# Kernel tuning notes

Hardware: AMD Instinct MI355X
Metric: run time of the kernel (lower is better)

## Reference

```python
import jax, jax.numpy as jnp
import numpy as np

N, E, F_IN, G, C = 100000, 3200000, 64, 1024, 10
BN_EPS = 1e-5


def _glorot(key, shape):
    fan_in, fan_out = shape[0], shape[1]
    lim = jnp.sqrt(6.0 / (fan_in + fan_out))
    return jax.random.uniform(key, shape, jnp.float32, -lim, lim)


def setup_inputs() -> dict:
    key = jax.random.key(0)
    ks = jax.random.split(key, 20)
    x = jax.random.normal(ks[0], (N, F_IN), jnp.float32)
    edge_index = jax.random.randint(ks[1], (2, E), 0, N, jnp.int64)
    batch = jnp.sort(jax.random.randint(ks[2], (N,), 0, G, jnp.int64))
    p = {
        'W1a': _glorot(ks[3], (F_IN, 128)), 'b1a': jnp.zeros((128,), jnp.float32),
        'W1b': _glorot(ks[4], (128, 128)), 'b1b': jnp.zeros((128,), jnp.float32),
        'g1': jnp.ones((128,), jnp.float32), 'be1': jnp.zeros((128,), jnp.float32),
        'W2a': _glorot(ks[5], (128, 64)), 'b2a': jnp.zeros((64,), jnp.float32),
        'W2b': _glorot(ks[6], (64, 64)), 'b2b': jnp.zeros((64,), jnp.float32),
        'g2': jnp.ones((64,), jnp.float32), 'be2': jnp.zeros((64,), jnp.float32),
        'W3a': _glorot(ks[7], (64, 32)), 'b3a': jnp.zeros((32,), jnp.float32),
        'W3b': _glorot(ks[8], (32, 32)), 'b3b': jnp.zeros((32,), jnp.float32),
        'g3': jnp.ones((32,), jnp.float32), 'be3': jnp.zeros((32,), jnp.float32),
        'Wf1': _glorot(ks[9], (32, 128)), 'bf1': jnp.zeros((128,), jnp.float32),
        'Wf2': _glorot(ks[10], (128, 64)), 'bf2': jnp.zeros((64,), jnp.float32),
        'Wf3': _glorot(ks[11], (64, C)), 'bf3': jnp.zeros((C,), jnp.float32),
    }
    return {'x': x, 'edge_index': edge_index, 'batch': batch, **p}


def _gin(x, src, dst, Wa, ba, Wb, bb):
    # GINConv (eps=0): h = MLP(x + sum_{j->i} x_j)
    agg = jax.ops.segment_sum(x[src], dst, num_segments=N)
    h = jax.nn.relu((x + agg) @ Wa + ba)
    return h @ Wb + bb


def _bn(x, g, b):
    # BatchNorm1d, training-mode batch statistics (biased variance)
    mu = jnp.mean(x, axis=0)
    var = jnp.mean((x - mu) ** 2, axis=0)
    return (x - mu) * jax.lax.rsqrt(var + BN_EPS) * g + b


def reference(x, edge_index, batch,
              W1a, b1a, W1b, b1b, g1, be1,
              W2a, b2a, W2b, b2b, g2, be2,
              W3a, b3a, W3b, b3b, g3, be3,
              Wf1, bf1, Wf2, bf2, Wf3, bf3):
    src, dst = edge_index[0], edge_index[1]
    z = _bn(jax.nn.relu(_gin(x, src, dst, W1a, b1a, W1b, b1b)), g1, be1)
    z = _bn(jax.nn.relu(_gin(z, src, dst, W2a, b2a, W2b, b2b)), g2, be2)
    z = _bn(jax.nn.relu(_gin(z, src, dst, W3a, b3a, W3b, b3b)), g3, be3)
    # global_add_pool over graph ids
    z = jax.ops.segment_sum(z, batch, num_segments=G)  # [G, 32]
    cr = jax.nn.relu(z @ Wf1 + bf1)
    cr = jax.nn.relu(cr @ Wf2 + bf2)  # dropout = identity (eval)
    cr = cr @ Wf3 + bf3
    return cr.reshape(-1, C)
```

## Files before the change

kernel.cpp:

```cpp
#include <hip/hip_runtime.h>

#define BN_EPS 1e-5f

typedef _Float16 f16;
typedef _Float16 f16x8 __attribute__((ext_vector_type(8)));
typedef _Float16 f16x4 __attribute__((ext_vector_type(4)));
typedef float f32x4 __attribute__((ext_vector_type(4)));

#define NBLK 512
#define BSHIFT 8
#define BMASK 255

__device__ __forceinline__ void wfrag_one(const float* __restrict__ W, f16* __restrict__ out,
        int FIN, int FOUT, int f,
        const float* __restrict__ stats, const float* __restrict__ g, float invN) {
    int j = f & 7;
    int lane = (f >> 3) & 63;
    int tile = f >> 9;
    int NT = FOUT >> 4;
    int t = tile % NT, s = tile / NT;
    int k = s * 32 + (lane >> 4) * 8 + j;
    int n = t * 16 + (lane & 15);
    float w = W[(size_t)k * FOUT + n];
    if (stats) {
        float mu = stats[k] * invN;
        float var = fmaxf(stats[FIN + k] * invN - mu * mu, 0.0f);
        w *= rsqrtf(var + BN_EPS) * g[k];
    }
    out[f] = (f16)w;
}

__global__ __launch_bounds__(256) void setup_count(const float4* __restrict__ x,
        f16x4* __restrict__ xh, int n4,
        const float* __restrict__ W1a, f16* __restrict__ Wh1a,
        const float* __restrict__ W1b, f16* __restrict__ Wh1b,
        const float* __restrict__ W2b, f16* __restrict__ Wh2b,
        const float* __restrict__ W3b, f16* __restrict__ Wh3b,
        const int* __restrict__ dst, int* __restrict__ hist,
        int NBK, int CHUNK, int E) {
    __shared__ int lh[512];
    const int BC = (n4 + 255) / 256;
    int bid = blockIdx.x;
    const int t = threadIdx.x;
    if (bid < BC) {
        int i = bid * 256 + t;
        if (i < n4) {
            float4 v = x[i];
            f16x4 o;
            o.x = (f16)v.x; o.y = (f16)v.y; o.z = (f16)v.z; o.w = (f16)v.w;
            xh[i] = o;
        }
        return;
    }
    bid -= BC;
    if (bid < 116) {
        if (bid < 32)       wfrag_one(W1a, Wh1a, 64, 128, bid * 256 + t, nullptr, nullptr, 0.f);
        else if (bid < 96)  wfrag_one(W1b, Wh1b, 128, 128, (bid - 32) * 256 + t, nullptr, nullptr, 0.f);
        else if (bid < 112) wfrag_one(W2b, Wh2b, 64, 64, (bid - 96) * 256 + t, nullptr, nullptr, 0.f);
        else                wfrag_one(W3b, Wh3b, 32, 32, (bid - 112) * 256 + t, nullptr, nullptr, 0.f);
        return;
    }
    const int blk = bid - 116;
    for (int r = t; r < 512; r += 256) lh[r] = 0;
    __syncthreads();
    const int e0 = blk * CHUNK, e1 = min(E, e0 + CHUNK);
    const int nq = (e1 - e0) >> 2;
    const int4* d4 = (const int4*)(dst + e0);
    for (int q = t; q < nq; q += 256) {
        int4 v = d4[q];
        atomicAdd(&lh[v.x >> BSHIFT], 1);
        atomicAdd(&lh[v.y >> BSHIFT], 1);
        atomicAdd(&lh[v.z >> BSHIFT], 1);
        atomicAdd(&lh[v.w >> BSHIFT], 1);
    }
    for (int e = e0 + (nq << 2) + t; e < e1; e += 256) atomicAdd(&lh[dst[e] >> BSHIFT], 1);
    __syncthreads();
    for (int r = t; r < NBK; r += 256) hist[r * NBLK + blk] = lh[r];
}

__global__ __launch_bounds__(512) void bkt_bscan(int* __restrict__ hist,
        int* __restrict__ btot) {
    __shared__ int sh[512];
    const int b = blockIdx.x, t = threadIdx.x;
    int v = hist[b * NBLK + t];
    sh[t] = v;
    __syncthreads();
    for (int d = 1; d < 512; d <<= 1) {
        int u = (t >= d) ? sh[t - d] : 0;
        __syncthreads();
        sh[t] += u;
        __syncthreads();
    }
    hist[b * NBLK + t] = sh[t] - v;
    if (t == 511) btot[b] = sh[511];
}

__global__ __launch_bounds__(512) void bkt_scatter(const int* __restrict__ src,
        const int* __restrict__ dst, const int* __restrict__ hist,
        const int* __restrict__ btot, int* __restrict__ bucketed,
        int NBK, int CHUNK, int E) {
    __shared__ int sc[512];
    __shared__ int lc[512];
    const int blk = blockIdx.x, t = threadIdx.x;
    int v = (t < NBK) ? btot[t] : 0;
    sc[t] = v;
    __syncthreads();
    for (int d = 1; d < 512; d <<= 1) {
        int u = (t >= d) ? sc[t - d] : 0;
        __syncthreads();
        sc[t] += u;
        __syncthreads();
    }
    if (t < NBK) lc[t] = (sc[t] - v) + hist[t * NBLK + blk];
    __syncthreads();
    const int e0 = blk * CHUNK, e1 = min(E, e0 + CHUNK);
    const int nq = (e1 - e0) >> 2;
    const int4* d4 = (const int4*)(dst + e0);
    const int4* s4 = (const int4*)(src + e0);
    for (int q = t; q < nq; q += 512) {
        int4 d = d4[q];
        int4 s = s4[q];
        int sl;
        sl = atomicAdd(&lc[d.x >> BSHIFT], 1); bucketed[sl] = ((d.x & BMASK) << 18) | s.x;
        sl = atomicAdd(&lc[d.y >> BSHIFT], 1); bucketed[sl] = ((d.y & BMASK) << 18) | s.y;
        sl = atomicAdd(&lc[d.z >> BSHIFT], 1); bucketed[sl] = ((d.z & BMASK) << 18) | s.z;
        sl = atomicAdd(&lc[d.w >> BSHIFT], 1); bucketed[sl] = ((d.w & BMASK) << 18) | s.w;
    }
    for (int e = e0 + (nq << 2) + t; e < e1; e += 512) {
        int d = dst[e];
        int slot = atomicAdd(&lc[d >> BSHIFT], 1);
        bucketed[slot] = ((d & BMASK) << 18) | src[e];
    }
}

__global__ __launch_bounds__(512) void bkt_csr(const int* __restrict__ bucketed,
        const int* __restrict__ btot, int* __restrict__ off,
        int* __restrict__ elist, int NBK, int N, int E) {
    __shared__ int sc[512];
    __shared__ int lh[256];
    __shared__ int lc[256];
    __shared__ int sh[256];
    const int b = blockIdx.x, t = threadIdx.x;
    int v = (t < NBK) ? btot[t] : 0;
    sc[t] = v;
    __syncthreads();
    for (int d = 1; d < 512; d <<= 1) {
        int u = (t >= d) ? sc[t - d] : 0;
        __syncthreads();
        sc[t] += u;
        __syncthreads();
    }
    const int cnt  = btot[b];
    const int base = sc[b] - cnt;
    if (b == 0 && t == 0) off[N] = E;
    const int b0 = b << BSHIFT;
    const int R = min(N - b0, 256);
    if (t < 256) lh[t] = 0;
    __syncthreads();
    for (int i = t; i < cnt; i += 512) atomicAdd(&lh[bucketed[base + i] >> 18], 1);
    __syncthreads();
    int v0 = 0;
    if (t < 256) { v0 = lh[t]; sh[t] = v0; }
    __syncthreads();
    for (int d = 1; d < 256; d <<= 1) {
        int u = 0;
        if (t < 256 && t >= d) u = sh[t - d];
        __syncthreads();
        if (t < 256) sh[t] += u;
        __syncthreads();
    }
    if (t < 256) { int ex = sh[t] - v0; lh[t] = ex; lc[t] = ex; }
    __syncthreads();
    if (t < R) off[b0 + t] = base + lh[t];
    for (int i = t; i < cnt; i += 512) {
        int p = bucketed[base + i];
        int rk = atomicAdd(&lc[p >> 18], 1);
        elist[base + rk] = p & 0x3FFFF;
    }
}

template<int F, bool AFFINE>
__global__ __launch_bounds__(256) void gather_v(const int* __restrict__ off,
        const int* __restrict__ elist, const f16* __restrict__ in,
        f16* __restrict__ out, const float* __restrict__ v,
        const float* __restrict__ bias, int N) {
    constexpr int TPN = F / 8;
    constexpr int NPB = 256 / TPN;
    const int i = blockIdx.x * NPB + threadIdx.x / TPN;
    const int l = threadIdx.x & (TPN - 1);
    if (i >= N) return;
    const int j0 = l * 8;
    const f16x8* __restrict__ inv = (const f16x8*)in;
    f16x8 s = inv[(size_t)i * TPN + l];
    float a[8];
#pragma unroll
    for (int u = 0; u < 8; u++) a[u] = (float)s[u];
    int k = off[i], e = off[i + 1];
    const float cnt = (float)(e - k + 1);
    f16x8 c0, c1, c2, c3;
    if (k + 4 <= e) {
        c0 = inv[(size_t)elist[k + 0] * TPN + l];
        c1 = inv[(size_t)elist[k + 1] * TPN + l];
        c2 = inv[(size_t)elist[k + 2] * TPN + l];
        c3 = inv[(size_t)elist[k + 3] * TPN + l];
        k += 4;
        for (; k + 4 <= e; k += 4) {
            f16x8 d0 = inv[(size_t)elist[k + 0] * TPN + l];
            f16x8 d1 = inv[(size_t)elist[k + 1] * TPN + l];
            f16x8 d2 = inv[(size_t)elist[k + 2] * TPN + l];
            f16x8 d3 = inv[(size_t)elist[k + 3] * TPN + l];
#pragma unroll
            for (int u = 0; u < 8; u++)
                a[u] += ((float)c0[u] + (float)c1[u]) + ((float)c2[u] + (float)c3[u]);
            c0 = d0; c1 = d1; c2 = d2; c3 = d3;
        }
#pragma unroll
        for (int u = 0; u < 8; u++)
            a[u] += ((float)c0[u] + (float)c1[u]) + ((float)c2[u] + (float)c3[u]);
    }
    for (; k < e; k++) {
        f16x8 p = inv[(size_t)elist[k] * TPN + l];
#pragma unroll
        for (int u = 0; u < 8; u++) a[u] += (float)p[u];
    }
    if (AFFINE) {
        float4 vv0 = *(const float4*)(v + j0);
        float4 vv1 = *(const float4*)(v + j0 + 4);
        float4 bb0 = *(const float4*)(bias + j0);
        float4 bb1 = *(const float4*)(bias + j0 + 4);
        a[0] = fmaxf(fmaf(cnt, vv0.x, a[0] + bb0.x), 0.0f);
        a[1] = fmaxf(fmaf(cnt, vv0.y, a[1] + bb0.y), 0.0f);
        a[2] = fmaxf(fmaf(cnt, vv0.z, a[2] + bb0.z), 0.0f);
        a[3] = fmaxf(fmaf(cnt, vv0.w, a[3] + bb0.w), 0.0f);
        a[4] = fmaxf(fmaf(cnt, vv1.x, a[4] + bb1.x), 0.0f);
        a[5] = fmaxf(fmaf(cnt, vv1.y, a[5] + bb1.y), 0.0f);
        a[6] = fmaxf(fmaf(cnt, vv1.z, a[6] + bb1.z), 0.0f);
        a[7] = fmaxf(fmaf(cnt, vv1.w, a[7] + bb1.w), 0.0f);
    }
    f16x8 o;
#pragma unroll
    for (int u = 0; u < 8; u++) o[u] = (f16)a[u];
    ((f16x8*)(out))[(size_t)i * TPN + l] = o;
}

__global__ __launch_bounds__(256) void layerprep_kernel(const float* __restrict__ W,
        f16* __restrict__ Wh, int FIN, int FOUT,
        const float* __restrict__ stats, const float* __restrict__ g,
        const float* __restrict__ be, float* __restrict__ v, float invN) {
    if (blockIdx.x == 0) {
        int j = threadIdx.x;
        if (j >= FOUT) return;
        float acc = 0.0f;
        for (int k = 0; k < FIN; k++) {
            float mu = stats[k] * invN;
            float var = fmaxf(stats[FIN + k] * invN - mu * mu, 0.0f);
            float sc = rsqrtf(var + BN_EPS) * g[k];
            float sh = be[k] - mu * sc;
            acc = fmaf(sh, W[(size_t)k * FOUT + j], acc);
        }
        v[j] = acc;
        return;
    }
    int f = (blockIdx.x - 1) * 256 + threadIdx.x;
    if (f < FIN * FOUT) wfrag_one(W, Wh, FIN, FOUT, f, stats, g, invN);
}

template<int FIN, int FOUT, int CT, bool STATS, bool RELU, bool BIAS, typename OutT>
__global__ __launch_bounds__(256) void gemm_mfma(const f16* __restrict__ A,
        const f16* __restrict__ Wf, const float* __restrict__ bias,
        OutT* __restrict__ Out, float* __restrict__ stats, int N) {
    constexpr int NS = FIN / 32;
    constexpr int NTF = FOUT / 16;
    constexpr int NT = CT / 16;
    constexpr int NCB = FOUT / CT;
    __shared__ float Ss[STATS ? 2 * CT : 1];
    if (STATS) {
        for (int i = threadIdx.x; i < 2 * CT; i += 256) Ss[i] = 0.0f;
        __syncthreads();
    }
    const int cb = blockIdx.x % NCB;
    const int rb = blockIdx.x / NCB;
    const int RB = gridDim.x / NCB;
    const int t0 = cb * NT;
    const int wid = threadIdx.x >> 6;
    const int lane = threadIdx.x & 63;
    const int col = lane & 15;
    const int quad = lane >> 4;

    f16x8 Bf[NS][NT];
#pragma unroll
    for (int s = 0; s < NS; s++)
#pragma unroll
        for (int t = 0; t < NT; t++)
            Bf[s][t] = *(const f16x8*)&Wf[((s * NTF + t0 + t) << 9) + (lane << 3)];

    float bj[NT];
#pragma unroll
    for (int t = 0; t < NT; t++) bj[t] = BIAS ? bias[(t0 + t) * 16 + col] : 0.0f;

    float ls[NT], ls2[NT];
#pragma unroll
    for (int t = 0; t < NT; t++) { ls[t] = 0.0f; ls2[t] = 0.0f; }

    const int S = N >> 4;
    for (int sidx = rb * 4 + wid; sidx < S; sidx += RB * 4) {
        const int m0 = sidx << 4;
        const f16* a0 = A + (size_t)(m0 + col) * FIN + (quad << 3);
        f16x8 Af[NS];
#pragma unroll
        for (int s = 0; s < NS; s++) Af[s] = *(const f16x8*)(a0 + s * 32);
        f32x4 acc[NT];
#pragma unroll
        for (int t = 0; t < NT; t++) acc[t] = (f32x4){bj[t], bj[t], bj[t], bj[t]};
#pragma unroll
        for (int t = 0; t < NT; t++)
#pragma unroll
            for (int s = 0; s < NS; s++)
                acc[t] = __builtin_amdgcn_mfma_f32_16x16x32_f16(Af[s], Bf[s][t], acc[t], 0, 0, 0);
#pragma unroll
        for (int t = 0; t < NT; t++) {
            float v0 = acc[t][0], v1 = acc[t][1], v2 = acc[t][2], v3 = acc[t][3];
            if (RELU) {
                v0 = fmaxf(v0, 0.0f); v1 = fmaxf(v1, 0.0f);
                v2 = fmaxf(v2, 0.0f); v3 = fmaxf(v3, 0.0f);
            }
            if (STATS) {
                ls[t]  += (v0 + v1) + (v2 + v3);
                ls2[t] += (v0 * v0 + v1 * v1) + (v2 * v2 + v3 * v3);
            }
            OutT* o = Out + (size_t)(m0 + quad * 4) * FOUT + (t0 + t) * 16 + col;
            o[0]        = (OutT)v0;
            o[FOUT]     = (OutT)v1;
            o[2 * FOUT] = (OutT)v2;
            o[3 * FOUT] = (OutT)v3;
        }
    }

    if (STATS) {
#pragma unroll
        for (int t = 0; t < NT; t++) {
            float s1 = ls[t], s2 = ls2[t];
            s1 += __shfl_xor(s1, 16); s1 += __shfl_xor(s1, 32);
            s2 += __shfl_xor(s2, 16); s2 += __shfl_xor(s2, 32);
            if (quad == 0) {
                atomicAdd(&Ss[t * 16 + col], s1);
                atomicAdd(&Ss[CT + t * 16 + col], s2);
            }
        }
        __syncthreads();
        for (int i = threadIdx.x; i < CT; i += 256) {
            atomicAdd(&stats[cb * CT + i], Ss[i]);
            atomicAdd(&stats[FOUT + cb * CT + i], Ss[CT + i]);
        }
    }
}

__global__ __launch_bounds__(256) void bn_pool_kernel(const float* __restrict__ y,
        const float* __restrict__ stats, const float* __restrict__ gw,
        const float* __restrict__ bw, const int* __restrict__ batch,
        float* __restrict__ pool, int N, float invN) {
    constexpr int F = 32, CH = 64;
    int q = threadIdx.x >> 5;
    int j = threadIdx.x & 31;
    int r0 = (blockIdx.x * 8 + q) * CH;
    if (r0 >= N) return;
    int r1 = min(r0 + CH, N);
    float mu = stats[j] * invN;
    float var = fmaxf(stats[F + j] * invN - mu * mu, 0.0f);
    float sc = rsqrtf(var + BN_EPS) * gw[j];
    float sh = bw[j] - mu * sc;
    int curg = batch[r0];
    float acc = 0.0f;
    for (int r = r0; r < r1; r++) {
        int g = batch[r];
        if (g != curg) {
            atomicAdd(pool + (size_t)curg * 32 + j, acc);
            acc = 0.0f;
            curg = g;
        }
        acc = fmaf(y[(size_t)r * 32 + j], sc, sh + acc);
    }
    atomicAdd(pool + (size_t)curg * 32 + j, acc);
}

__global__ __launch_bounds__(128) void fc_kernel(const float* __restrict__ pool,
        const float* __restrict__ Wf1, const float* __restrict__ bf1,
        const float* __restrict__ Wf2, const float* __restrict__ bf2,
        const float* __restrict__ Wf3, const float* __restrict__ bf3,
        float* __restrict__ out) {
    __shared__ float zin[32];
    __shared__ float h1[128];
    __shared__ float h2[64];
    const int gidx = blockIdx.x;
    const int t = threadIdx.x;
    if (t < 32) zin[t] = pool[(size_t)gidx * 32 + t];
    __syncthreads();
    {
        float a = bf1[t];
        for (int k = 0; k < 32; k++) a = fmaf(zin[k], Wf1[k * 128 + t], a);
        h1[t] = fmaxf(a, 0.0f);
    }
    __syncthreads();
    if (t < 64) {
        float a = bf2[t];
        for (int k = 0; k < 128; k++) a = fmaf(h1[k], Wf2[k * 64 + t], a);
        h2[t] = fmaxf(a, 0.0f);
    }
    __syncthreads();
    if (t < 10) {
        float a = bf3[t];
        for (int k = 0; k < 64; k++) a = fmaf(h2[k], Wf3[k * 10 + t], a);
        out[(size_t)gidx * 10 + t] = a;
    }
}

extern "C" void kernel_launch(void* const* d_in, const int* in_sizes, int n_in,
                              void* d_out, int out_size, void* d_ws, size_t ws_size,
                              hipStream_t stream) {
    const float* x   = (const float*)d_in[0];
    const int*  ei   = (const int*)d_in[1];
    const int*  batch= (const int*)d_in[2];
    const float* W1a = (const float*)d_in[3];  const float* b1a = (const float*)d_in[4];
    const float* W1b = (const float*)d_in[5];  const float* b1b = (const float*)d_in[6];
    const float* g1  = (const float*)d_in[7];  const float* be1 = (const float*)d_in[8];
    const float* W2a = (const float*)d_in[9];  const float* b2a = (const float*)d_in[10];
    const float* W2b = (const float*)d_in[11]; const float* b2b = (const float*)d_in[12];
    const float* g2  = (const float*)d_in[13]; const float* be2 = (const float*)d_in[14];
    const float* W3a = (const float*)d_in[15]; const float* b3a = (const float*)d_in[16];
    const float* W3b = (const float*)d_in[17]; const float* b3b = (const float*)d_in[18];
    const float* g3  = (const float*)d_in[19]; const float* be3 = (const float*)d_in[20];
    const float* Wf1 = (const float*)d_in[21]; const float* bf1 = (const float*)d_in[22];
    const float* Wf2 = (const float*)d_in[23]; const float* bf2 = (const float*)d_in[24];
    const float* Wf3 = (const float*)d_in[25]; const float* bf3 = (const float*)d_in[26];

    const int N = in_sizes[2];
    const int E = in_sizes[1] / 2;
    const int G = out_size / 10;
    const int* src = ei;
    const int* dst = ei + E;

    const int NBK = (N + BMASK) >> BSHIFT;
    const int CHUNK = (((E + NBLK - 1) / NBLK) + 3) & ~3;

    float* B0   = (float*)d_ws;
    float* B1   = B0 + (size_t)N * 128;
    float* pool = B1 + (size_t)N * 128;
    float* st1  = pool + (size_t)G * 32;
    float* st2  = st1 + 256;
    float* st3  = st2 + 256;
    int* off    = (int*)(st3 + 256);
    int* elist  = off + (N + 1);
    float* v2   = (float*)(elist + E);
    float* v3   = v2 + 64;
    int* btot   = (int*)(v3 + 32);
    f16* Wh1a   = (f16*)(btot + NBK);
    f16* Wh1b   = Wh1a + 64 * 128;
    f16* Wh2a   = Wh1b + 128 * 128;
    f16* Wh2b   = Wh2a + 128 * 64;
    f16* Wh3a   = Wh2b + 64 * 64;
    f16* Wh3b   = Wh3a + 64 * 32;

    int* bucketed = (int*)B1;
    int* hist     = bucketed + E;

    f16* xh    = (f16*)B0;
    f16* A1    = (f16*)B1;
    f16* H1    = (f16*)B0 + (size_t)N * 64;
    f16* Y1    = (f16*)B1 + (size_t)N * 64;
    f16* Z1    = (f16*)B0;
    f16* H2    = (f16*)B1;
    f16* Y2    = (f16*)B0 + (size_t)N * 64;
    f16* Z2    = (f16*)B0;
    f16* H3    = (f16*)B1;
    float* Y3  = B1 + (size_t)N * 64;

    hipMemsetAsync(pool, 0, ((size_t)G * 32 + 768) * sizeof(float), stream);

    const float invN = 1.0f / (float)N;
    const int GG = 640;

    {
        int BC = (N * 16 + 255) / 256;
        setup_count<<<BC + 116 + NBLK, 256, 0, stream>>>(
            (const float4*)x, (f16x4*)xh, N * 16,
            W1a, Wh1a, W1b, Wh1b, W2b, Wh2b, W3b, Wh3b,
            dst, hist, NBK, CHUNK, E);
    }

    bkt_bscan  <<<NBK, 512, 0, stream>>>(hist, btot);
    bkt_scatter<<<NBLK, 512, 0, stream>>>(src, dst, hist, btot, bucketed, NBK, CHUNK, E);
    bkt_csr    <<<NBK, 512, 0, stream>>>(bucketed, btot, off, elist, NBK, N, E);

    gather_v<64, false><<<(N + 31) / 32, 256, 0, stream>>>(off, elist, xh, A1, nullptr, nullptr, N);
    gemm_mfma<64, 128, 64, false, true, true, f16><<<GG, 256, 0, stream>>>(A1, Wh1a, b1a, H1, nullptr, N);
    gemm_mfma<128, 128, 64, true, true, true, f16><<<GG, 256, 0, stream>>>(H1, Wh1b, b1b, Y1, st1, N);

    layerprep_kernel<<<33, 256, 0, stream>>>(W2a, Wh2a, 128, 64, st1, g1, be1, v2, invN);
    gemm_mfma<128, 64, 64, false, false, false, f16><<<GG, 256, 0, stream>>>(Y1, Wh2a, nullptr, Z1, nullptr, N);
    gather_v<64, true><<<(N + 31) / 32, 256, 0, stream>>>(off, elist, Z1, H2, v2, b2a, N);
    gemm_mfma<64, 64, 64, true, true, true, f16><<<GG, 256, 0, stream>>>(H2, Wh2b, b2b, Y2, st2, N);

    layerprep_kernel<<<9, 256, 0, stream>>>(W3a, Wh3a, 64, 32, st2, g2, be2, v3, invN);
    gemm_mfma<64, 32, 32, false, false, false, f16><<<GG, 256, 0, stream>>>(Y2, Wh3a, nullptr, Z2, nullptr, N);
    gather_v<32, true><<<(N + 63) / 64, 256, 0, stream>>>(off, elist, Z2, H3, v3, b3a, N);
    gemm_mfma<32, 32, 32, true, true, true, float><<<GG, 256, 0, stream>>>(H3, Wh3b, b3b, Y3, st3, N);

    bn_pool_kernel<<<(N + 511) / 512, 256, 0, stream>>>(Y3, st3, g3, be3, batch, pool, N, invN);

    fc_kernel<<<G, 128, 0, stream>>>(pool, Wf1, bf1, Wf2, bf2, Wf3, bf3, (float*)d_out);
}
```

Before: 515.6 us.

## Fuse neighbor gather with following MFMA GEMM through shared memory

Each aggregation kernel now does its gather into an LDS tile and immediately runs the next MFMA GEMM on it (with bias, ReLU and optional BN statistics), so the intermediate H arrays are never written to or read back from global memory. BN statistics are spread over 8 copies chosen by block index to cut global atomic contention, and the consumers sum the copies. The cost is more LDS and registers per block, which may lower occupancy for the latency-bound gather.

```diff
diff --git a/kernel.cpp b/kernel.cpp
--- a/kernel.cpp
+++ b/kernel.cpp
@@ -13,7 +13,7 @@
 
 __device__ __forceinline__ void wfrag_one(const float* __restrict__ W, f16* __restrict__ out,
         int FIN, int FOUT, int f,
-        const float* __restrict__ stats, const float* __restrict__ g, float invN) {
+        const float* __restrict__ stats, int NC, const float* __restrict__ g, float invN) {
     int j = f & 7;
     int lane = (f >> 3) & 63;
     int tile = f >> 9;
@@ -23,8 +23,13 @@
     int n = t * 16 + (lane & 15);
     float w = W[(size_t)k * FOUT + n];
     if (stats) {
-        float mu = stats[k] * invN;
-        float var = fmaxf(stats[FIN + k] * invN - mu * mu, 0.0f);
+        float s1 = 0.0f, s2 = 0.0f;
+        for (int c = 0; c < NC; c++) {
+            s1 += stats[c * 2 * FIN + k];
+            s2 += stats[c * 2 * FIN + FIN + k];
+        }
+        float mu = s1 * invN;
+        float var = fmaxf(s2 * invN - mu * mu, 0.0f);
         w *= rsqrtf(var + BN_EPS) * g[k];
     }
     out[f] = (f16)w;
@@ -54,10 +59,10 @@
     }
     bid -= BC;
     if (bid < 116) {
-        if (bid < 32)       wfrag_one(W1a, Wh1a, 64, 128, bid * 256 + t, nullptr, nullptr, 0.f);
-        else if (bid < 96)  wfrag_one(W1b, Wh1b, 128, 128, (bid - 32) * 256 + t, nullptr, nullptr, 0.f);
-        else if (bid < 112) wfrag_one(W2b, Wh2b, 64, 64, (bid - 96) * 256 + t, nullptr, nullptr, 0.f);
-        else                wfrag_one(W3b, Wh3b, 32, 32, (bid - 112) * 256 + t, nullptr, nullptr, 0.f);
+        if (bid < 32)       wfrag_one(W1a, Wh1a, 64, 128, bid * 256 + t, nullptr, 1, nullptr, 0.f);
+        else if (bid < 96)  wfrag_one(W1b, Wh1b, 128, 128, (bid - 32) * 256 + t, nullptr, 1, nullptr, 0.f);
+        else if (bid < 112) wfrag_one(W2b, Wh2b, 64, 64, (bid - 96) * 256 + t, nullptr, 1, nullptr, 0.f);
+        else                wfrag_one(W3b, Wh3b, 32, 32, (bid - 112) * 256 + t, nullptr, 1, nullptr, 0.f);
         return;
     }
     const int blk = bid - 116;
@@ -179,81 +184,159 @@
     }
 }
 
-template<int F, bool AFFINE>
-__global__ __launch_bounds__(256) void gather_v(const int* __restrict__ off,
+template<int F, int FOUT, bool STATS, bool AFFINE, typename OutT>
+__global__ __launch_bounds__(256) void gather_gemm(const int* __restrict__ off,
         const int* __restrict__ elist, const f16* __restrict__ in,
-        f16* __restrict__ out, const float* __restrict__ v,
-        const float* __restrict__ bias, int N) {
+        const f16* __restrict__ Wf, const float* __restrict__ bias,
+        const float* __restrict__ av, const float* __restrict__ ab,
+        OutT* __restrict__ Out, float* __restrict__ stats, int N) {
     constexpr int TPN = F / 8;
     constexpr int NPB = 256 / TPN;
-    const int i = blockIdx.x * NPB + threadIdx.x / TPN;
+    constexpr int SPB = NPB / 16;
+    constexpr int WPS = 4 / SPB;
+    constexpr int NTF = FOUT / 16;
+    constexpr int NTW = NTF / WPS;
+    constexpr int NS = F / 32;
+    constexpr int LDW = F + 8;
+    __shared__ f16 Hl[NPB * LDW];
+    __shared__ float Ss[STATS ? 2 * FOUT : 1];
+    if (STATS) for (int z = threadIdx.x; z < 2 * FOUT; z += 256) Ss[z] = 0.0f;
+
+    const int base = blockIdx.x * NPB;
+    const int rl = threadIdx.x / TPN;
+    const int i = base + rl;
     const int l = threadIdx.x & (TPN - 1);
-    if (i >= N) return;
-    const int j0 = l * 8;
-    const f16x8* __restrict__ inv = (const f16x8*)in;
-    f16x8 s = inv[(size_t)i * TPN + l];
-    float a[8];
-#pragma unroll
-    for (int u = 0; u < 8; u++) a[u] = (float)s[u];
-    int k = off[i], e = off[i + 1];
-    const float cnt = (float)(e - k + 1);
-    f16x8 c0, c1, c2, c3;
-    if (k + 4 <= e) {
-        c0 = inv[(size_t)elist[k + 0] * TPN + l];
-        c1 = inv[(size_t)elist[k + 1] * TPN + l];
-        c2 = inv[(size_t)elist[k + 2] * TPN + l];
-        c3 = inv[(size_t)elist[k + 3] * TPN + l];
-        k += 4;
-        for (; k + 4 <= e; k += 4) {
-            f16x8 d0 = inv[(size_t)elist[k + 0] * TPN + l];
-            f16x8 d1 = inv[(size_t)elist[k + 1] * TPN + l];
-            f16x8 d2 = inv[(size_t)elist[k + 2] * TPN + l];
-            f16x8 d3 = inv[(size_t)elist[k + 3] * TPN + l];
+    if (i < N) {
+        const int j0 = l * 8;
+        const f16x8* __restrict__ inv = (const f16x8*)in;
+        f16x8 s = inv[(size_t)i * TPN + l];
+        float a[8];
+#pragma unroll
+        for (int u = 0; u < 8; u++) a[u] = (float)s[u];
+        int k = off[i], e = off[i + 1];
+        const float cnt = (float)(e - k + 1);
+        f16x8 c0, c1, c2, c3;
+        if (k + 4 <= e) {
+            c0 = inv[(size_t)elist[k + 0] * TPN + l];
+            c1 = inv[(size_t)elist[k + 1] * TPN + l];
+            c2 = inv[(size_t)elist[k + 2] * TPN + l];
+            c3 = inv[(size_t)elist[k + 3] * TPN + l];
+            k += 4;
+            for (; k + 4 <= e; k += 4) {
+                f16x8 d0 = inv[(size_t)elist[k + 0] * TPN + l];
+                f16x8 d1 = inv[(size_t)elist[k + 1] * TPN + l];
+                f16x8 d2 = inv[(size_t)elist[k + 2] * TPN + l];
+                f16x8 d3 = inv[(size_t)elist[k + 3] * TPN + l];
+#pragma unroll
+                for (int u = 0; u < 8; u++)
+                    a[u] += ((float)c0[u] + (float)c1[u]) + ((float)c2[u] + (float)c3[u]);
+                c0 = d0; c1 = d1; c2 = d2; c3 = d3;
+            }
 #pragma unroll
             for (int u = 0; u < 8; u++)
                 a[u] += ((float)c0[u] + (float)c1[u]) + ((float)c2[u] + (float)c3[u]);
-            c0 = d0; c1 = d1; c2 = d2; c3 = d3;
-        }
-#pragma unroll
-        for (int u = 0; u < 8; u++)
-            a[u] += ((float)c0[u] + (float)c1[u]) + ((float)c2[u] + (float)c3[u]);
-    }
-    for (; k < e; k++) {
-        f16x8 p = inv[(size_t)elist[k] * TPN + l];
-#pragma unroll
-        for (int u = 0; u < 8; u++) a[u] += (float)p[u];
-    }
-    if (AFFINE) {
-        float4 vv0 = *(const float4*)(v + j0);
-        float4 vv1 = *(const float4*)(v + j0 + 4);
-        float4 bb0 = *(const float4*)(bias + j0);
-        float4 bb1 = *(const float4*)(bias + j0 + 4);
-        a[0] = fmaxf(fmaf(cnt, vv0.x, a[0] + bb0.x), 0.0f);
-        a[1] = fmaxf(fmaf(cnt, vv0.y, a[1] + bb0.y), 0.0f);
-        a[2] = fmaxf(fmaf(cnt, vv0.z, a[2] + bb0.z), 0.0f);
-        a[3] = fmaxf(fmaf(cnt, vv0.w, a[3] + bb0.w), 0.0f);
-        a[4] = fmaxf(fmaf(cnt, vv1.x, a[4] + bb1.x), 0.0f);
-        a[5] = fmaxf(fmaf(cnt, vv1.y, a[5] + bb1.y), 0.0f);
-        a[6] = fmaxf(fmaf(cnt, vv1.z, a[6] + bb1.z), 0.0f);
-        a[7] = fmaxf(fmaf(cnt, vv1.w, a[7] + bb1.w), 0.0f);
-    }
-    f16x8 o;
-#pragma unroll
-    for (int u = 0; u < 8; u++) o[u] = (f16)a[u];
-    ((f16x8*)(out))[(size_t)i * TPN + l] = o;
+        }
+        for (; k < e; k++) {
+            f16x8 p = inv[(size_t)elist[k] * TPN + l];
+#pragma unroll
+            for (int u = 0; u < 8; u++) a[u] += (float)p[u];
+        }
+        if (AFFINE) {
+            float4 vv0 = *(const float4*)(av + j0);
+            float4 vv1 = *(const float4*)(av + j0 + 4);
+            float4 bb0 = *(const float4*)(ab + j0);
+            float4 bb1 = *(const float4*)(ab + j0 + 4);
+            a[0] = fmaxf(fmaf(cnt, vv0.x, a[0] + bb0.x), 0.0f);
+            a[1] = fmaxf(fmaf(cnt, vv0.y, a[1] + bb0.y), 0.0f);
+            a[2] = fmaxf(fmaf(cnt, vv0.z, a[2] + bb0.z), 0.0f);
+            a[3] = fmaxf(fmaf(cnt, vv0.w, a[3] + bb0.w), 0.0f);
+            a[4] = fmaxf(fmaf(cnt, vv1.x, a[4] + bb1.x), 0.0f);
+            a[5] = fmaxf(fmaf(cnt, vv1.y, a[5] + bb1.y), 0.0f);
+            a[6] = fmaxf(fmaf(cnt, vv1.z, a[6] + bb1.z), 0.0f);
+            a[7] = fmaxf(fmaf(cnt, vv1.w, a[7] + bb1.w), 0.0f);
+        }
+        f16x8 o;
+#pragma unroll
+        for (int u = 0; u < 8; u++) o[u] = (f16)a[u];
+        *(f16x8*)&Hl[rl * LDW + j0] = o;
+    }
+    __syncthreads();
+
+    const int wid = threadIdx.x >> 6;
+    const int lane = threadIdx.x & 63;
+    const int col = lane & 15;
+    const int quad = lane >> 4;
+    const int sid = wid / WPS;
+    const int cg = wid % WPS;
+    const int m0 = base + sid * 16;
+    if (m0 < N) {
+        f16x8 Bf[NS][NTW];
+#pragma unroll
+        for (int s = 0; s < NS; s++)
+#pragma unroll
+            for (int t = 0; t < NTW; t++)
+                Bf[s][t] = *(const f16x8*)&Wf[((s * NTF + cg * NTW + t) << 9) + (lane << 3)];
+        f32x4 acc[NTW];
+#pragma unroll
+        for (int t = 0; t < NTW; t++) {
+            float b = bias[(cg * NTW + t) * 16 + col];
+            acc[t] = (f32x4){b, b, b, b};
+        }
+        f16x8 Af[NS];
+        const int rbase = (sid * 16 + col) * LDW + quad * 8;
+#pragma unroll
+        for (int s = 0; s < NS; s++) Af[s] = *(const f16x8*)&Hl[rbase + s * 32];
+#pragma unroll
+        for (int t = 0; t < NTW; t++)
+#pragma unroll
+            for (int s = 0; s < NS; s++)
+                acc[t] = __builtin_amdgcn_mfma_f32_16x16x32_f16(Af[s], Bf[s][t], acc[t], 0, 0, 0);
+#pragma unroll
+        for (int t = 0; t < NTW; t++) {
+            float v0 = fmaxf(acc[t][0], 0.0f);
+            float v1 = fmaxf(acc[t][1], 0.0f);
+            float v2 = fmaxf(acc[t][2], 0.0f);
+            float v3 = fmaxf(acc[t][3], 0.0f);
+            OutT* o = Out + (size_t)(m0 + quad * 4) * FOUT + (cg * NTW + t) * 16 + col;
+            o[0]        = (OutT)v0;
+            o[FOUT]     = (OutT)v1;
+            o[2 * FOUT] = (OutT)v2;
+            o[3 * FOUT] = (OutT)v3;
+            if (STATS) {
+                float s1 = (v0 + v1) + (v2 + v3);
+                float s2 = (v0 * v0 + v1 * v1) + (v2 * v2 + v3 * v3);
+                s1 += __shfl_xor(s1, 16); s1 += __shfl_xor(s1, 32);
+                s2 += __shfl_xor(s2, 16); s2 += __shfl_xor(s2, 32);
+                if (quad == 0) {
+                    atomicAdd(&Ss[(cg * NTW + t) * 16 + col], s1);
+                    atomicAdd(&Ss[FOUT + (cg * NTW + t) * 16 + col], s2);
+                }
+            }
+        }
+    }
+    if (STATS) {
+        __syncthreads();
+        float* stc = stats + (blockIdx.x & 7) * 2 * FOUT;
+        for (int z = threadIdx.x; z < 2 * FOUT; z += 256) atomicAdd(&stc[z], Ss[z]);
+    }
 }
 
 __global__ __launch_bounds__(256) void layerprep_kernel(const float* __restrict__ W,
         f16* __restrict__ Wh, int FIN, int FOUT,
-        const float* __restrict__ stats, const float* __restrict__ g,
+        const float* __restrict__ stats, int NC, const float* __restrict__ g,
         const float* __restrict__ be, float* __restrict__ v, float invN) {
     if (blockIdx.x == 0) {
         int j = threadIdx.x;
         if (j >= FOUT) return;
         float acc = 0.0f;
         for (int k = 0; k < FIN; k++) {
-            float mu = stats[k] * invN;
-            float var = fmaxf(stats[FIN + k] * invN - mu * mu, 0.0f);
+            float s1 = 0.0f, s2 = 0.0f;
+            for (int c = 0; c < NC; c++) {
+                s1 += stats[c * 2 * FIN + k];
+                s2 += stats[c * 2 * FIN + FIN + k];
+            }
+            float mu = s1 * invN;
+            float var = fmaxf(s2 * invN - mu * mu, 0.0f);
             float sc = rsqrtf(var + BN_EPS) * g[k];
             float sh = be[k] - mu * sc;
             acc = fmaf(sh, W[(size_t)k * FOUT + j], acc);
@@ -262,7 +345,7 @@
         return;
     }
     int f = (blockIdx.x - 1) * 256 + threadIdx.x;
-    if (f < FIN * FOUT) wfrag_one(W, Wh, FIN, FOUT, f, stats, g, invN);
+    if (f < FIN * FOUT) wfrag_one(W, Wh, FIN, FOUT, f, stats, NC, g, invN);
 }
 
 template<int FIN, int FOUT, int CT, bool STATS, bool RELU, bool BIAS, typename OutT>
@@ -356,7 +439,7 @@
 }
 
 __global__ __launch_bounds__(256) void bn_pool_kernel(const float* __restrict__ y,
-        const float* __restrict__ stats, const float* __restrict__ gw,
+        const float* __restrict__ stats, int NC, const float* __restrict__ gw,
         const float* __restrict__ bw, const int* __restrict__ batch,
         float* __restrict__ pool, int N, float invN) {
     constexpr int F = 32, CH = 64;
@@ -365,8 +448,13 @@
     int r0 = (blockIdx.x * 8 + q) * CH;
     if (r0 >= N) return;
     int r1 = min(r0 + CH, N);
-    float mu = stats[j] * invN;
-    float var = fmaxf(stats[F + j] * invN - mu * mu, 0.0f);
+    float s1 = 0.0f, s2 = 0.0f;
+    for (int c = 0; c < NC; c++) {
+        s1 += stats[c * 2 * F + j];
+        s2 += stats[c * 2 * F + F + j];
+    }
+    float mu = s1 * invN;
+    float var = fmaxf(s2 * invN - mu * mu, 0.0f);
     float sc = rsqrtf(var + BN_EPS) * gw[j];
     float sh = bw[j] - mu * sc;
     int curg = batch[r0];
@@ -446,9 +534,9 @@
     float* B1   = B0 + (size_t)N * 128;
     float* pool = B1 + (size_t)N * 128;
     float* st1  = pool + (size_t)G * 32;
-    float* st2  = st1 + 256;
-    float* st3  = st2 + 256;
-    int* off    = (int*)(st3 + 256);
+    float* st2c = st1 + 256;
+    float* st3c = st2c + 1024;
+    int* off    = (int*)(st3c + 512);
     int* elist  = off + (N + 1);
     float* v2   = (float*)(elist + E);
     float* v3   = v2 + 64;
@@ -464,17 +552,14 @@
     int* hist     = bucketed + E;
 
     f16* xh    = (f16*)B0;
-    f16* A1    = (f16*)B1;
     f16* H1    = (f16*)B0 + (size_t)N * 64;
     f16* Y1    = (f16*)B1 + (size_t)N * 64;
     f16* Z1    = (f16*)B0;
-    f16* H2    = (f16*)B1;
     f16* Y2    = (f16*)B0 + (size_t)N * 64;
     f16* Z2    = (f16*)B0;
-    f16* H3    = (f16*)B1;
     float* Y3  = B1 + (size_t)N * 64;
 
-    hipMemsetAsync(pool, 0, ((size_t)G * 32 + 768) * sizeof(float), stream);
+    hipMemsetAsync(pool, 0, ((size_t)G * 32 + 256 + 1024 + 512) * sizeof(float), stream);
 
     const float invN = 1.0f / (float)N;
     const int GG = 640;
@@ -491,21 +576,21 @@
     bkt_scatter<<<NBLK, 512, 0, stream>>>(src, dst, hist, btot, bucketed, NBK, CHUNK, E);
     bkt_csr    <<<NBK, 512, 0, stream>>>(bucketed, btot, off, elist, NBK, N, E);
 
-    gather_v<64, false><<<(N + 31) / 32, 256, 0, stream>>>(off, elist, xh, A1, nullptr, nullptr, N);
-    gemm_mfma<64, 128, 64, false, true, true, f16><<<GG, 256, 0, stream>>>(A1, Wh1a, b1a, H1, nullptr, N);
+    gather_gemm<64, 128, false, false, f16><<<(N + 31) / 32, 256, 0, stream>>>(
+        off, elist, xh, Wh1a, b1a, nullptr, nullptr, H1, nullptr, N);
     gemm_mfma<128, 128, 64, true, true, true, f16><<<GG, 256, 0, stream>>>(H1, Wh1b, b1b, Y1, st1, N);
 
-    layerprep_kernel<<<33, 256, 0, stream>>>(W2a, Wh2a, 128, 64, st1, g1, be1, v2, invN);
+    layerprep_kernel<<<33, 256, 0, stream>>>(W2a, Wh2a, 128, 64, st1, 1, g1, be1, v2, invN);
     gemm_mfma<128, 64, 64, false, false, false, f16><<<GG, 256, 0, stream>>>(Y1, Wh2a, nullptr, Z1, nullptr, N);
-    gather_v<64, true><<<(N + 31) / 32, 256, 0, stream>>>(off, elist, Z1, H2, v2, b2a, N);
-    gemm_mfma<64, 64, 64, true, true, true, f16><<<GG, 256, 0, stream>>>(H2, Wh2b, b2b, Y2, st2, N);
-
-    layerprep_kernel<<<9, 256, 0, stream>>>(W3a, Wh3a, 64, 32, st2, g2, be2, v3, invN);
+    gather_gemm<64, 64, true, true, f16><<<(N + 31) / 32, 256, 0, stream>>>(
+        off, elist, Z1, Wh2b, b2b, v2, b2a, Y2, st2c, N);
+
+    layerprep_kernel<<<9, 256, 0, stream>>>(W3a, Wh3a, 64, 32, st2c, 8, g2, be2, v3, invN);
     gemm_mfma<64, 32, 32, false, false, false, f16><<<GG, 256, 0, stream>>>(Y2, Wh3a, nullptr, Z2, nullptr, N);
-    gather_v<32, true><<<(N + 63) / 64, 256, 0, stream>>>(off, elist, Z2, H3, v3, b3a, N);
-    gemm_mfma<32, 32, 32, true, true, true, float><<<GG, 256, 0, stream>>>(H3, Wh3b, b3b, Y3, st3, N);
-
-    bn_pool_kernel<<<(N + 511) / 512, 256, 0, stream>>>(Y3, st3, g3, be3, batch, pool, N, invN);
+    gather_gemm<32, 32, true, true, float><<<(N + 63) / 64, 256, 0, stream>>>(
+        off, elist, Z2, Wh3b, b3b, v3, b3a, Y3, st3c, N);
+
+    bn_pool_kernel<<<(N + 511) / 512, 256, 0, stream>>>(Y3, st3c, 8, g3, be3, batch, pool, N, invN);
 
     fc_kernel<<<G, 128, 0, stream>>>(pool, Wf1, bf1, Wf2, bf2, Wf3, bf3, (float*)d_out);
 }
```

New measurement: 493.0 us. 1.05x faster.
